# Performance work log

Measured on AMD Instinct MI355X. Metric: run time of the kernel, lower is better.

The kernel has to match this reference:

```python
import jax, jax.numpy as jnp
import numpy as np

B, T, C, H = 8, 2048, 1024, 128

def setup_inputs() -> dict:
    key = jax.random.key(0)
    k1, k2, k3, k4 = jax.random.split(key, 4)
    scale = 0.02
    return {
        "x": jax.random.normal(k1, (B, T, C), dtype=jnp.float32),
        "Wq": jax.random.normal(k2, (C, H), dtype=jnp.float32) * scale,
        "Wk": jax.random.normal(k3, (C, H), dtype=jnp.float32) * scale,
        "Wv": jax.random.normal(k4, (C, H), dtype=jnp.float32) * scale,
    }

def reference(x, Wq, Wk, Wv):
    # Single causal attention head (dropout p=0.0 -> identity)
    q = jnp.einsum('btc,ch->bth', x, Wq)
    k = jnp.einsum('btc,ch->bth', x, Wk)
    v = jnp.einsum('btc,ch->bth', x, Wv)
    head_size = k.shape[-1]
    scores = jnp.einsum('bth,bsh->bts', q, k) / jnp.sqrt(jnp.asarray(head_size, q.dtype))  # [B,T,T]
    causal = jnp.tril(jnp.ones((scores.shape[1], scores.shape[2]), dtype=bool))
    scores = jnp.where(causal, scores, -jnp.inf)
    weights = jax.nn.softmax(scores, axis=-1)
    context = jnp.einsum('bts,bsh->bth', weights, v)  # [B,T,H]
    return context
```

## Files before the change

### kernel.cpp

```cpp
#include <hip/hip_runtime.h>

typedef __bf16 bf16x8 __attribute__((ext_vector_type(8)));
typedef float f32x4 __attribute__((ext_vector_type(4)));
typedef float fv4 __attribute__((ext_vector_type(4)));

#define B_ 8
#define T_ 2048
#define C_ 1024
#define H_ 128

__global__ __launch_bounds__(256) void prep_kernel(
    const float* __restrict__ Wq, const float* __restrict__ Wk,
    const float* __restrict__ Wv, __bf16* __restrict__ Wt)
{
  __shared__ __bf16 ldsT[128 * 136];
  const int tid = threadIdx.x;
  const int k0 = blockIdx.x * 128;
  const int wsel = blockIdx.y;
  const float* W = wsel == 0 ? Wq : (wsel == 1 ? Wk : Wv);
#pragma unroll
  for (int i = 0; i < 16; ++i) {
    int fidx = tid + 256 * i;
    int k = fidx >> 5, h4 = (fidx & 31) << 2;
    fv4 w = *(const fv4*)(W + (size_t)(k0 + k) * H_ + h4);
#pragma unroll
    for (int j = 0; j < 4; ++j) ldsT[(h4 + j) * 136 + k] = (__bf16)w[j];
  }
  __syncthreads();
#pragma unroll
  for (int i = 0; i < 8; ++i) {
    int sidx = tid + 256 * i;
    int h = sidx >> 4, c8 = (sidx & 15) << 3;
    *(bf16x8*)(Wt + (size_t)wsel * H_ * C_ + (size_t)h * C_ + k0 + c8) =
        *(const bf16x8*)&ldsT[h * 136 + c8];
  }
}

__global__ __launch_bounds__(256) void proj_kernel(
    const float* __restrict__ x, const __bf16* __restrict__ Wt,
    __bf16* __restrict__ Qw, __bf16* __restrict__ Kw, __bf16* __restrict__ Vtw)
{
  __shared__ __align__(16) __bf16 smem[128 * 136];
  __bf16* ldsA = smem;
  __bf16* ldsB = smem + 5120;
  const int tid = threadIdx.x;
  const int wave = tid >> 6;
  const int lane = tid & 63;
  const int q4 = lane >> 4;
  const int l16 = lane & 15;
  const int wsel = blockIdx.y;
  const int bt0 = blockIdx.x * 128;
  const __bf16* Wb = Wt + (size_t)wsel * H_ * C_;

  const f32x4 zero4 = {0.f, 0.f, 0.f, 0.f};
  f32x4 acc[2][8];
#pragma unroll
  for (int mt = 0; mt < 2; ++mt)
#pragma unroll
    for (int nt = 0; nt < 8; ++nt) acc[mt][nt] = zero4;

  fv4 xa[2][2];
  bf16x8 wb[2];
#pragma unroll
  for (int i = 0; i < 2; ++i) {
    int idx = tid + 256 * i;
    int row = idx >> 2, col8 = (idx & 3) << 3;
    const float* s = x + (size_t)(bt0 + row) * C_ + col8;
    xa[i][0] = *(const fv4*)s;
    xa[i][1] = *(const fv4*)(s + 4);
    wb[i] = *(const bf16x8*)(Wb + (size_t)row * C_ + col8);
  }

  for (int kc = 0; kc < C_; kc += 32) {
#pragma unroll
    for (int i = 0; i < 2; ++i) {
      int idx = tid + 256 * i;
      int row = idx >> 2, col8 = (idx & 3) << 3;
      bf16x8 v;
#pragma unroll
      for (int j = 0; j < 4; ++j) { v[j] = (__bf16)xa[i][0][j]; v[4 + j] = (__bf16)xa[i][1][j]; }
      *(bf16x8*)&ldsA[row * 40 + col8] = v;
      *(bf16x8*)&ldsB[row * 40 + col8] = wb[i];
    }
    __syncthreads();
    int kn = (kc + 32 < C_) ? kc + 32 : kc;
#pragma unroll
    for (int i = 0; i < 2; ++i) {
      int idx = tid + 256 * i;
      int row = idx >> 2, col8 = (idx & 3) << 3;
      const float* s = x + (size_t)(bt0 + row) * C_ + kn + col8;
      xa[i][0] = *(const fv4*)s;
      xa[i][1] = *(const fv4*)(s + 4);
      wb[i] = *(const bf16x8*)(Wb + (size_t)row * C_ + kn + col8);
    }
    bf16x8 af[2];
#pragma unroll
    for (int mt = 0; mt < 2; ++mt)
      af[mt] = *(const bf16x8*)&ldsA[(wave * 32 + mt * 16 + l16) * 40 + q4 * 8];
#pragma unroll
    for (int nt = 0; nt < 8; ++nt) {
      bf16x8 bf = *(const bf16x8*)&ldsB[(nt * 16 + l16) * 40 + q4 * 8];
#pragma unroll
      for (int mt = 0; mt < 2; ++mt)
        acc[mt][nt] = __builtin_amdgcn_mfma_f32_16x16x32_bf16(af[mt], bf, acc[mt][nt], 0, 0, 0);
    }
    __syncthreads();
  }

  if (wsel != 2) {
    __bf16* dst = (wsel == 0) ? Qw : Kw;
#pragma unroll
    for (int mt = 0; mt < 2; ++mt)
#pragma unroll
      for (int nt = 0; nt < 8; ++nt)
#pragma unroll
        for (int r = 0; r < 4; ++r) {
          int row = bt0 + wave * 32 + mt * 16 + q4 * 4 + r;
          dst[(size_t)row * H_ + nt * 16 + l16] = (__bf16)acc[mt][nt][r];
        }
  } else {
#pragma unroll
    for (int mt = 0; mt < 2; ++mt)
#pragma unroll
      for (int nt = 0; nt < 8; ++nt)
#pragma unroll
        for (int r = 0; r < 4; ++r) {
          int tl = wave * 32 + mt * 16 + q4 * 4 + r;
          int h = nt * 16 + l16;
          smem[h * 136 + tl] = (__bf16)acc[mt][nt][r];
        }
    __syncthreads();
    const int b = bt0 >> 11, t0 = bt0 & (T_ - 1);
#pragma unroll
    for (int i = 0; i < 8; ++i) {
      int sidx = tid + 256 * i;
      int h = sidx >> 4, c8 = (sidx & 15) << 3;
      *(bf16x8*)(Vtw + ((size_t)b * H_ + h) * T_ + t0 + c8) =
          *(const bf16x8*)&smem[h * 136 + c8];
    }
  }
}

__global__ __launch_bounds__(256) void attn_kernel(
    const __bf16* __restrict__ Q, const __bf16* __restrict__ K,
    const __bf16* __restrict__ Vt, float* __restrict__ out)
{
  __shared__ __align__(16) __bf16 ldsK[64 * 136];
  __shared__ __align__(16) __bf16 ldsV[128 * 72];
  __shared__ __align__(16) __bf16 ldsP[4][16 * 72];
  const int tid = threadIdx.x;
  const int wave = tid >> 6;
  const int lane = tid & 63;
  const int q4 = lane >> 4, l16 = lane & 15;
  const int qb = blockIdx.x, b = blockIdx.y;
  const int q0 = qb * 64;
  const int qw = q0 + wave * 16;
  const __bf16* Qb = Q + (size_t)b * T_ * H_;
  const __bf16* Kb = K + (size_t)b * T_ * H_;
  const __bf16* Vb = Vt + (size_t)b * H_ * T_;
  __bf16* ldsPw = &ldsP[wave][0];

  bf16x8 qf[4];
#pragma unroll
  for (int kc = 0; kc < 4; ++kc)
    qf[kc] = *(const bf16x8*)(Qb + (size_t)(qw + l16) * H_ + kc * 32 + q4 * 8);

  const f32x4 zero4 = {0.f, 0.f, 0.f, 0.f};
  f32x4 o[8];
#pragma unroll
  for (int nt = 0; nt < 8; ++nt) o[nt] = zero4;
  float lsum[4] = {0.f, 0.f, 0.f, 0.f};

  const int ntile = qb + 1;

  bf16x8 kp[4], vp[4];
#pragma unroll
  for (int i = 0; i < 4; ++i) {
    int idx = tid + 256 * i;
    int krow = idx >> 4, kcol8 = (idx & 15) << 3;
    kp[i] = *(const bf16x8*)(Kb + (size_t)krow * H_ + kcol8);
    int vrow = idx >> 3, vcol8 = (idx & 7) << 3;
    vp[i] = *(const bf16x8*)(Vb + (size_t)vrow * T_ + vcol8);
  }

  for (int t = 0; t < ntile; ++t) {
    const int kv0 = t << 6;
#pragma unroll
    for (int i = 0; i < 4; ++i) {
      int idx = tid + 256 * i;
      int krow = idx >> 4, kcol8 = (idx & 15) << 3;
      *(bf16x8*)&ldsK[krow * 136 + kcol8] = kp[i];
      int vrow = idx >> 3, vcol8 = (idx & 7) << 3;
      *(bf16x8*)&ldsV[vrow * 72 + vcol8] = vp[i];
    }
    __syncthreads();
    int kvn = (t + 1 < ntile) ? (kv0 + 64) : kv0;
#pragma unroll
    for (int i = 0; i < 4; ++i) {
      int idx = tid + 256 * i;
      int krow = idx >> 4, kcol8 = (idx & 15) << 3;
      kp[i] = *(const bf16x8*)(Kb + (size_t)(kvn + krow) * H_ + kcol8);
      int vrow = idx >> 3, vcol8 = (idx & 7) << 3;
      vp[i] = *(const bf16x8*)(Vb + (size_t)vrow * T_ + kvn + vcol8);
    }

    f32x4 s[4];
#pragma unroll
    for (int nt = 0; nt < 4; ++nt) s[nt] = zero4;
#pragma unroll
    for (int nt = 0; nt < 4; ++nt)
#pragma unroll
      for (int kc = 0; kc < 4; ++kc) {
        bf16x8 kf = *(const bf16x8*)&ldsK[(nt * 16 + l16) * 136 + kc * 32 + q4 * 8];
        s[nt] = __builtin_amdgcn_mfma_f32_16x16x32_bf16(qf[kc], kf, s[nt], 0, 0, 0);
      }

#pragma unroll
    for (int r = 0; r < 4; ++r) {
      const int grow = qw + q4 * 4 + r;
#pragma unroll
      for (int nt = 0; nt < 4; ++nt) {
        int col = kv0 + nt * 16 + l16;
        float p = (col <= grow) ? __expf(s[nt][r] * 0.08838834764831845f) : 0.f;
        lsum[r] += p;
        ldsPw[(q4 * 4 + r) * 72 + nt * 16 + l16] = (__bf16)p;
      }
    }
#pragma unroll
    for (int kc2 = 0; kc2 < 2; ++kc2) {
      bf16x8 pf = *(const bf16x8*)&ldsPw[l16 * 72 + kc2 * 32 + q4 * 8];
#pragma unroll
      for (int nt = 0; nt < 8; ++nt) {
        bf16x8 vf = *(const bf16x8*)&ldsV[(nt * 16 + l16) * 72 + kc2 * 32 + q4 * 8];
        o[nt] = __builtin_amdgcn_mfma_f32_16x16x32_bf16(pf, vf, o[nt], 0, 0, 0);
      }
    }
    __syncthreads();
  }

  float rinv[4];
#pragma unroll
  for (int r = 0; r < 4; ++r) {
    float l = lsum[r];
    l += __shfl_xor(l, 1);
    l += __shfl_xor(l, 2);
    l += __shfl_xor(l, 4);
    l += __shfl_xor(l, 8);
    rinv[r] = 1.f / l;
  }
#pragma unroll
  for (int nt = 0; nt < 8; ++nt)
#pragma unroll
    for (int r = 0; r < 4; ++r) {
      int row = qw + q4 * 4 + r;
      out[((size_t)b * T_ + row) * H_ + nt * 16 + l16] = o[nt][r] * rinv[r];
    }
}

extern "C" void kernel_launch(void* const* d_in, const int* in_sizes, int n_in,
                              void* d_out, int out_size, void* d_ws, size_t ws_size,
                              hipStream_t stream) {
  const float* x  = (const float*)d_in[0];
  const float* Wq = (const float*)d_in[1];
  const float* Wk = (const float*)d_in[2];
  const float* Wv = (const float*)d_in[3];
  __bf16* ws = (__bf16*)d_ws;
  __bf16* Qw  = ws;
  __bf16* Kw  = ws + (size_t)B_ * T_ * H_;
  __bf16* Vtw = ws + (size_t)2 * B_ * T_ * H_;
  __bf16* Wt  = ws + (size_t)3 * B_ * T_ * H_;
  float* out = (float*)d_out;

  prep_kernel<<<dim3(8, 3), 256, 0, stream>>>(Wq, Wk, Wv, Wt);
  proj_kernel<<<dim3(128, 3), 256, 0, stream>>>(x, Wt, Qw, Kw, Vtw);
  attn_kernel<<<dim3(32, 8), 256, 0, stream>>>(Qw, Kw, Vtw, out);
}
```

Measured before the change: 183.9 us.

## Split causal attention over KV chunks and fuse QKV projection into one GEMM

The projection kernel now computes Q, K and V together in one block: 32 rows of x against all 384 weight columns. x is therefore read and converted once instead of three times. Attention for long query blocks is split into chunks of 8 KV tiles, which balances the causal triangle across 640 blocks instead of 256 uneven ones. The partial numerators and denominators are written to workspace and summed by a combine kernel. This relies on the exponentials being unnormalised with no running max, and a fallback kernel runs when the workspace is too small.

New measurement: 174.2 us. 1.06x faster.

```diff
diff --git a/kernel.cpp b/kernel.cpp
--- a/kernel.cpp
+++ b/kernel.cpp
@@ -40,108 +40,282 @@
     const float* __restrict__ x, const __bf16* __restrict__ Wt,
     __bf16* __restrict__ Qw, __bf16* __restrict__ Kw, __bf16* __restrict__ Vtw)
 {
-  __shared__ __align__(16) __bf16 smem[128 * 136];
-  __bf16* ldsA = smem;
-  __bf16* ldsB = smem + 5120;
+  __shared__ __align__(16) __bf16 ldsA[32 * 40];
+  __shared__ __align__(16) __bf16 ldsB[384 * 40];
   const int tid = threadIdx.x;
-  const int wave = tid >> 6;
-  const int lane = tid & 63;
-  const int q4 = lane >> 4;
-  const int l16 = lane & 15;
-  const int wsel = blockIdx.y;
-  const int bt0 = blockIdx.x * 128;
-  const __bf16* Wb = Wt + (size_t)wsel * H_ * C_;
+  const int wave = tid >> 6, lane = tid & 63;
+  const int q4 = lane >> 4, l16 = lane & 15;
+  const int bt0 = blockIdx.x * 32;
 
   const f32x4 zero4 = {0.f, 0.f, 0.f, 0.f};
-  f32x4 acc[2][8];
+  f32x4 acc[2][6];
 #pragma unroll
   for (int mt = 0; mt < 2; ++mt)
 #pragma unroll
-    for (int nt = 0; nt < 8; ++nt) acc[mt][nt] = zero4;
-
-  fv4 xa[2][2];
-  bf16x8 wb[2];
+    for (int nt = 0; nt < 6; ++nt) acc[mt][nt] = zero4;
+
+  fv4 xa0, xa1;
+  bf16x8 wpre[6];
+  const int arow = tid >> 2, acol8 = (tid & 3) << 3;
+  if (tid < 128) {
+    const float* s = x + (size_t)(bt0 + arow) * C_ + acol8;
+    xa0 = *(const fv4*)s;
+    xa1 = *(const fv4*)(s + 4);
+  }
+#pragma unroll
+  for (int i = 0; i < 6; ++i) {
+    int idx = tid + 256 * i;
+    int col = idx >> 2, k8 = (idx & 3) << 3;
+    wpre[i] = *(const bf16x8*)(Wt + (size_t)col * C_ + k8);
+  }
+
+  for (int kc = 0; kc < C_; kc += 32) {
+    if (tid < 128) {
+      bf16x8 v;
+#pragma unroll
+      for (int j = 0; j < 4; ++j) { v[j] = (__bf16)xa0[j]; v[4 + j] = (__bf16)xa1[j]; }
+      *(bf16x8*)&ldsA[arow * 40 + acol8] = v;
+    }
+#pragma unroll
+    for (int i = 0; i < 6; ++i) {
+      int idx = tid + 256 * i;
+      int col = idx >> 2, k8 = (idx & 3) << 3;
+      *(bf16x8*)&ldsB[col * 40 + k8] = wpre[i];
+    }
+    __syncthreads();
+    const int kn = (kc + 32 < C_) ? kc + 32 : kc;
+    if (tid < 128) {
+      const float* s = x + (size_t)(bt0 + arow) * C_ + kn + acol8;
+      xa0 = *(const fv4*)s;
+      xa1 = *(const fv4*)(s + 4);
+    }
+#pragma unroll
+    for (int i = 0; i < 6; ++i) {
+      int idx = tid + 256 * i;
+      int col = idx >> 2, k8 = (idx & 3) << 3;
+      wpre[i] = *(const bf16x8*)(Wt + (size_t)col * C_ + kn + k8);
+    }
+    bf16x8 af[2];
+#pragma unroll
+    for (int mt = 0; mt < 2; ++mt)
+      af[mt] = *(const bf16x8*)&ldsA[(mt * 16 + l16) * 40 + q4 * 8];
+#pragma unroll
+    for (int nt = 0; nt < 6; ++nt) {
+      bf16x8 bf = *(const bf16x8*)&ldsB[(wave * 96 + nt * 16 + l16) * 40 + q4 * 8];
+#pragma unroll
+      for (int mt = 0; mt < 2; ++mt)
+        acc[mt][nt] = __builtin_amdgcn_mfma_f32_16x16x32_bf16(af[mt], bf, acc[mt][nt], 0, 0, 0);
+    }
+    __syncthreads();
+  }
+
+  const int b = bt0 >> 11, t0 = bt0 & (T_ - 1);
+#pragma unroll
+  for (int mt = 0; mt < 2; ++mt)
+#pragma unroll
+    for (int nt = 0; nt < 6; ++nt) {
+      int gcol = wave * 96 + nt * 16 + l16;
+#pragma unroll
+      for (int r = 0; r < 4; ++r) {
+        int row = bt0 + mt * 16 + q4 * 4 + r;
+        float v = acc[mt][nt][r];
+        if (gcol < 128) Qw[(size_t)row * H_ + gcol] = (__bf16)v;
+        else if (gcol < 256) Kw[(size_t)row * H_ + (gcol - 128)] = (__bf16)v;
+        else {
+          int tl = mt * 16 + q4 * 4 + r;
+          ldsB[(gcol - 256) * 40 + tl] = (__bf16)v;
+        }
+      }
+    }
+  __syncthreads();
 #pragma unroll
   for (int i = 0; i < 2; ++i) {
     int idx = tid + 256 * i;
-    int row = idx >> 2, col8 = (idx & 3) << 3;
-    const float* s = x + (size_t)(bt0 + row) * C_ + col8;
-    xa[i][0] = *(const fv4*)s;
-    xa[i][1] = *(const fv4*)(s + 4);
-    wb[i] = *(const bf16x8*)(Wb + (size_t)row * C_ + col8);
-  }
-
-  for (int kc = 0; kc < C_; kc += 32) {
-#pragma unroll
-    for (int i = 0; i < 2; ++i) {
-      int idx = tid + 256 * i;
-      int row = idx >> 2, col8 = (idx & 3) << 3;
-      bf16x8 v;
-#pragma unroll
-      for (int j = 0; j < 4; ++j) { v[j] = (__bf16)xa[i][0][j]; v[4 + j] = (__bf16)xa[i][1][j]; }
-      *(bf16x8*)&ldsA[row * 40 + col8] = v;
-      *(bf16x8*)&ldsB[row * 40 + col8] = wb[i];
-    }
-    __syncthreads();
-    int kn = (kc + 32 < C_) ? kc + 32 : kc;
-#pragma unroll
-    for (int i = 0; i < 2; ++i) {
-      int idx = tid + 256 * i;
-      int row = idx >> 2, col8 = (idx & 3) << 3;
-      const float* s = x + (size_t)(bt0 + row) * C_ + kn + col8;
-      xa[i][0] = *(const fv4*)s;
-      xa[i][1] = *(const fv4*)(s + 4);
-      wb[i] = *(const bf16x8*)(Wb + (size_t)row * C_ + kn + col8);
-    }
-    bf16x8 af[2];
-#pragma unroll
-    for (int mt = 0; mt < 2; ++mt)
-      af[mt] = *(const bf16x8*)&ldsA[(wave * 32 + mt * 16 + l16) * 40 + q4 * 8];
-#pragma unroll
-    for (int nt = 0; nt < 8; ++nt) {
-      bf16x8 bf = *(const bf16x8*)&ldsB[(nt * 16 + l16) * 40 + q4 * 8];
-#pragma unroll
-      for (int mt = 0; mt < 2; ++mt)
-        acc[mt][nt] = __builtin_amdgcn_mfma_f32_16x16x32_bf16(af[mt], bf, acc[mt][nt], 0, 0, 0);
-    }
-    __syncthreads();
-  }
-
-  if (wsel != 2) {
-    __bf16* dst = (wsel == 0) ? Qw : Kw;
-#pragma unroll
-    for (int mt = 0; mt < 2; ++mt)
-#pragma unroll
-      for (int nt = 0; nt < 8; ++nt)
-#pragma unroll
-        for (int r = 0; r < 4; ++r) {
-          int row = bt0 + wave * 32 + mt * 16 + q4 * 4 + r;
-          dst[(size_t)row * H_ + nt * 16 + l16] = (__bf16)acc[mt][nt][r];
+    int h = idx >> 2, t8 = (idx & 3) << 3;
+    *(bf16x8*)(Vtw + ((size_t)b * H_ + h) * T_ + t0 + t8) =
+        *(const bf16x8*)&ldsB[h * 40 + t8];
+  }
+}
+
+__global__ __launch_bounds__(256) void attn_split(
+    const __bf16* __restrict__ Q, const __bf16* __restrict__ K,
+    const __bf16* __restrict__ Vt, float* __restrict__ PO,
+    float* __restrict__ Pl, float* __restrict__ out)
+{
+  __shared__ __align__(16) __bf16 ldsK[64 * 136];
+  __shared__ __align__(16) __bf16 ldsV[128 * 72];
+  __shared__ __align__(16) __bf16 ldsP[4][16 * 72];
+  const int tid = threadIdx.x;
+  const int wave = tid >> 6, lane = tid & 63;
+  const int q4 = lane >> 4, l16 = lane & 15;
+  const int b = blockIdx.y;
+  int rem = blockIdx.x, qb = 0;
+  while (rem >= (qb >> 3) + 1) { rem -= (qb >> 3) + 1; ++qb; }
+  const int c = rem;
+  const int tstart = c << 3;
+  const int tend = min(tstart + 8, qb + 1);
+  const int nch = (qb >> 3) + 1;
+  const int qw = qb * 64 + wave * 16;
+  const __bf16* Qb = Q + (size_t)b * T_ * H_;
+  const __bf16* Kb = K + (size_t)b * T_ * H_;
+  const __bf16* Vb = Vt + (size_t)b * H_ * T_;
+  __bf16* ldsPw = &ldsP[wave][0];
+
+  bf16x8 qf[4];
+#pragma unroll
+  for (int kc = 0; kc < 4; ++kc)
+    qf[kc] = *(const bf16x8*)(Qb + (size_t)(qw + l16) * H_ + kc * 32 + q4 * 8);
+
+  const f32x4 zero4 = {0.f, 0.f, 0.f, 0.f};
+  f32x4 o[8];
+#pragma unroll
+  for (int nt = 0; nt < 8; ++nt) o[nt] = zero4;
+  float lsum[4] = {0.f, 0.f, 0.f, 0.f};
+
+  bf16x8 kp[4], vp[4];
+#pragma unroll
+  for (int i = 0; i < 4; ++i) {
+    int idx = tid + 256 * i;
+    int krow = idx >> 4, kcol8 = (idx & 15) << 3;
+    kp[i] = *(const bf16x8*)(Kb + (size_t)(tstart * 64 + krow) * H_ + kcol8);
+    int vrow = idx >> 3, vcol8 = (idx & 7) << 3;
+    vp[i] = *(const bf16x8*)(Vb + (size_t)vrow * T_ + tstart * 64 + vcol8);
+  }
+
+  for (int t = tstart; t < tend; ++t) {
+    const int kv0 = t << 6;
+#pragma unroll
+    for (int i = 0; i < 4; ++i) {
+      int idx = tid + 256 * i;
+      int krow = idx >> 4, kcol8 = (idx & 15) << 3;
+      *(bf16x8*)&ldsK[krow * 136 + kcol8] = kp[i];
+      int vrow = idx >> 3, vcol8 = (idx & 7) << 3;
+      *(bf16x8*)&ldsV[vrow * 72 + vcol8] = vp[i];
+    }
+    __syncthreads();
+    const int kvn = (t + 1 < tend) ? (kv0 + 64) : kv0;
+#pragma unroll
+    for (int i = 0; i < 4; ++i) {
+      int idx = tid + 256 * i;
+      int krow = idx >> 4, kcol8 = (idx & 15) << 3;
+      kp[i] = *(const bf16x8*)(Kb + (size_t)(kvn + krow) * H_ + kcol8);
+      int vrow = idx >> 3, vcol8 = (idx & 7) << 3;
+      vp[i] = *(const bf16x8*)(Vb + (size_t)vrow * T_ + kvn + vcol8);
+    }
+
+    f32x4 s[4];
+#pragma unroll
+    for (int nt = 0; nt < 4; ++nt) s[nt] = zero4;
+#pragma unroll
+    for (int nt = 0; nt < 4; ++nt)
+#pragma unroll
+      for (int kc = 0; kc < 4; ++kc) {
+        bf16x8 kf = *(const bf16x8*)&ldsK[(nt * 16 + l16) * 136 + kc * 32 + q4 * 8];
+        s[nt] = __builtin_amdgcn_mfma_f32_16x16x32_bf16(qf[kc], kf, s[nt], 0, 0, 0);
+      }
+
+    if (t == qb) {
+#pragma unroll
+      for (int r = 0; r < 4; ++r) {
+        const int grow = qw + q4 * 4 + r;
+#pragma unroll
+        for (int nt = 0; nt < 4; ++nt) {
+          int col = kv0 + nt * 16 + l16;
+          float p = (col <= grow) ? __expf(s[nt][r] * 0.08838834764831845f) : 0.f;
+          lsum[r] += p;
+          ldsPw[(q4 * 4 + r) * 72 + nt * 16 + l16] = (__bf16)p;
         }
+      }
+    } else {
+#pragma unroll
+      for (int r = 0; r < 4; ++r)
+#pragma unroll
+        for (int nt = 0; nt < 4; ++nt) {
+          float p = __expf(s[nt][r] * 0.08838834764831845f);
+          lsum[r] += p;
+          ldsPw[(q4 * 4 + r) * 72 + nt * 16 + l16] = (__bf16)p;
+        }
+    }
+#pragma unroll
+    for (int kc2 = 0; kc2 < 2; ++kc2) {
+      bf16x8 pf = *(const bf16x8*)&ldsPw[l16 * 72 + kc2 * 32 + q4 * 8];
+#pragma unroll
+      for (int nt = 0; nt < 8; ++nt) {
+        bf16x8 vf = *(const bf16x8*)&ldsV[(nt * 16 + l16) * 72 + kc2 * 32 + q4 * 8];
+        o[nt] = __builtin_amdgcn_mfma_f32_16x16x32_bf16(pf, vf, o[nt], 0, 0, 0);
+      }
+    }
+    __syncthreads();
+  }
+
+  float lred[4];
+#pragma unroll
+  for (int r = 0; r < 4; ++r) {
+    float l = lsum[r];
+    l += __shfl_xor(l, 1);
+    l += __shfl_xor(l, 2);
+    l += __shfl_xor(l, 4);
+    l += __shfl_xor(l, 8);
+    lred[r] = l;
+  }
+
+  if (nch == 1) {
+#pragma unroll
+    for (int r = 0; r < 4; ++r) lred[r] = 1.f / lred[r];
+#pragma unroll
+    for (int nt = 0; nt < 8; ++nt)
+#pragma unroll
+      for (int r = 0; r < 4; ++r) {
+        int row = qw + q4 * 4 + r;
+        out[((size_t)b * T_ + row) * H_ + nt * 16 + l16] = o[nt][r] * lred[r];
+      }
   } else {
-#pragma unroll
-    for (int mt = 0; mt < 2; ++mt)
-#pragma unroll
-      for (int nt = 0; nt < 8; ++nt)
-#pragma unroll
-        for (int r = 0; r < 4; ++r) {
-          int tl = wave * 32 + mt * 16 + q4 * 4 + r;
-          int h = nt * 16 + l16;
-          smem[h * 136 + tl] = (__bf16)acc[mt][nt][r];
-        }
-    __syncthreads();
-    const int b = bt0 >> 11, t0 = bt0 & (T_ - 1);
-#pragma unroll
-    for (int i = 0; i < 8; ++i) {
-      int sidx = tid + 256 * i;
-      int h = sidx >> 4, c8 = (sidx & 15) << 3;
-      *(bf16x8*)(Vtw + ((size_t)b * H_ + h) * T_ + t0 + c8) =
-          *(const bf16x8*)&smem[h * 136 + c8];
-    }
-  }
-}
-
-__global__ __launch_bounds__(256) void attn_kernel(
+    const int slot = b * 80 + qb + max(qb - 8, 0) + max(qb - 16, 0) + max(qb - 24, 0) + c;
+    float* POs = PO + (size_t)slot * 8192;
+#pragma unroll
+    for (int nt = 0; nt < 8; ++nt)
+#pragma unroll
+      for (int r = 0; r < 4; ++r)
+        POs[(wave * 16 + q4 * 4 + r) * 128 + nt * 16 + l16] = o[nt][r];
+    if (l16 == 0)
+#pragma unroll
+      for (int r = 0; r < 4; ++r)
+        Pl[slot * 64 + wave * 16 + q4 * 4 + r] = lred[r];
+  }
+}
+
+__global__ __launch_bounds__(256) void attn_combine(
+    const float* __restrict__ PO, const float* __restrict__ Pl,
+    float* __restrict__ out)
+{
+  const int qb = blockIdx.x + 8;
+  const int b = blockIdx.y;
+  const int nch = (qb >> 3) + 1;
+  const int slot0 = b * 80 + qb + max(qb - 8, 0) + max(qb - 16, 0) + max(qb - 24, 0);
+  const int tid = threadIdx.x;
+  const int row = tid >> 2, h0 = (tid & 3) << 5;
+  const fv4 z4 = {0.f, 0.f, 0.f, 0.f};
+  fv4 oacc[8];
+#pragma unroll
+  for (int j = 0; j < 8; ++j) oacc[j] = z4;
+  float lacc = 0.f;
+  for (int cc = 0; cc < nch; ++cc) {
+    const int slot = slot0 + cc;
+    lacc += Pl[slot * 64 + row];
+    const float* Ps = PO + (size_t)slot * 8192 + row * 128 + h0;
+#pragma unroll
+    for (int j = 0; j < 8; ++j) oacc[j] += *(const fv4*)(Ps + 4 * j);
+  }
+  const float inv = 1.f / lacc;
+  float* op = out + ((size_t)b * T_ + qb * 64 + row) * H_ + h0;
+#pragma unroll
+  for (int j = 0; j < 8; ++j) {
+    fv4 v = oacc[j] * inv;
+    *(fv4*)(op + 4 * j) = v;
+  }
+}
+
+__global__ __launch_bounds__(256) void attn_mono(
     const __bf16* __restrict__ Q, const __bf16* __restrict__ K,
     const __bf16* __restrict__ Vt, float* __restrict__ out)
 {
@@ -149,12 +323,10 @@
   __shared__ __align__(16) __bf16 ldsV[128 * 72];
   __shared__ __align__(16) __bf16 ldsP[4][16 * 72];
   const int tid = threadIdx.x;
-  const int wave = tid >> 6;
-  const int lane = tid & 63;
+  const int wave = tid >> 6, lane = tid & 63;
   const int q4 = lane >> 4, l16 = lane & 15;
   const int qb = blockIdx.x, b = blockIdx.y;
-  const int q0 = qb * 64;
-  const int qw = q0 + wave * 16;
+  const int qw = qb * 64 + wave * 16;
   const __bf16* Qb = Q + (size_t)b * T_ * H_;
   const __bf16* Kb = K + (size_t)b * T_ * H_;
   const __bf16* Vb = Vt + (size_t)b * H_ * T_;
@@ -170,7 +342,6 @@
 #pragma unroll
   for (int nt = 0; nt < 8; ++nt) o[nt] = zero4;
   float lsum[4] = {0.f, 0.f, 0.f, 0.f};
-
   const int ntile = qb + 1;
 
   bf16x8 kp[4], vp[4];
@@ -203,7 +374,6 @@
       int vrow = idx >> 3, vcol8 = (idx & 7) << 3;
       vp[i] = *(const bf16x8*)(Vb + (size_t)vrow * T_ + kvn + vcol8);
     }
-
     f32x4 s[4];
 #pragma unroll
     for (int nt = 0; nt < 4; ++nt) s[nt] = zero4;
@@ -214,7 +384,6 @@
         bf16x8 kf = *(const bf16x8*)&ldsK[(nt * 16 + l16) * 136 + kc * 32 + q4 * 8];
         s[nt] = __builtin_amdgcn_mfma_f32_16x16x32_bf16(qf[kc], kf, s[nt], 0, 0, 0);
       }
-
 #pragma unroll
     for (int r = 0; r < 4; ++r) {
       const int grow = qw + q4 * 4 + r;
@@ -237,7 +406,6 @@
     }
     __syncthreads();
   }
-
   float rinv[4];
 #pragma unroll
   for (int r = 0; r < 4; ++r) {
@@ -269,9 +437,18 @@
   __bf16* Kw  = ws + (size_t)B_ * T_ * H_;
   __bf16* Vtw = ws + (size_t)2 * B_ * T_ * H_;
   __bf16* Wt  = ws + (size_t)3 * B_ * T_ * H_;
+  const size_t bf16_bytes = 13369344;
+  float* PO = (float*)((char*)d_ws + bf16_bytes);
+  float* Pl = PO + (size_t)640 * 64 * 128;
+  const size_t need = bf16_bytes + ((size_t)640 * 64 * 128 + 640 * 64) * 4;
   float* out = (float*)d_out;
 
   prep_kernel<<<dim3(8, 3), 256, 0, stream>>>(Wq, Wk, Wv, Wt);
-  proj_kernel<<<dim3(128, 3), 256, 0, stream>>>(x, Wt, Qw, Kw, Vtw);
-  attn_kernel<<<dim3(32, 8), 256, 0, stream>>>(Qw, Kw, Vtw, out);
-}
+  proj_kernel<<<512, 256, 0, stream>>>(x, Wt, Qw, Kw, Vtw);
+  if (ws_size >= need) {
+    attn_split<<<dim3(80, 8), 256, 0, stream>>>(Qw, Kw, Vtw, PO, Pl, out);
+    attn_combine<<<dim3(24, 8), 256, 0, stream>>>(PO, Pl, out);
+  } else {
+    attn_mono<<<dim3(32, 8), 256, 0, stream>>>(Qw, Kw, Vtw, out);
+  }
+}
```
